# Optimization experiments

Measured on AMD Instinct MI355X. Metric: run time of the kernel, lower is better.

## Reference

```python
import jax, jax.numpy as jnp
import numpy as np

B, S, D = 4, 4096, 2048  # batch, seq, hidden
E, R, K = 8, 16, 2       # n_experts, rank, top_k


def setup_inputs() -> dict:
    key = jax.random.key(0)
    k1, k2, k3, k4 = jax.random.split(key, 4)
    x = jax.random.normal(k1, (B, S, D), dtype=jnp.float32)
    router_w = jax.random.normal(k2, (E, D), dtype=jnp.float32) * 0.02  # nn.Linear weight (out,in)
    experts_down = jax.random.normal(k3, (E, D, R), dtype=jnp.float32) * 0.01
    experts_up = jax.random.normal(k4, (E, R, D), dtype=jnp.float32) * 0.01
    return {"x": x, "router_w": router_w, "experts_down": experts_down, "experts_up": experts_up}


def reference(x, router_w, experts_down, experts_up):
    E_ = router_w.shape[0]
    # router sees detached x (torch: self.router(x.detach()))
    logits = jnp.einsum('bsd,ed->bse', jax.lax.stop_gradient(x), router_w)
    w, idx = jax.lax.top_k(logits, K)          # (B,S,K)
    w = jax.nn.softmax(w, axis=-1)
    # combined per-token, per-expert routing weight; zero for non-selected experts
    w_full = jnp.sum(jax.nn.one_hot(idx, E_, dtype=x.dtype) * w[..., None], axis=2)  # (B,S,E)
    # rank-space activations per expert: (B,S,E,R) -- small (R=16)
    h = jnp.einsum('bsd,edr->bser', x, experts_down)
    # fuse routing weight into rank space, then up-project and sum over experts
    out = x + jnp.einsum('bser,bse,erd->bsd', h, w_full, experts_up)
    return out
```

## Files before the change

kernel.cpp:

```cpp
#include <hip/hip_runtime.h>
#include <hip/hip_bf16.h>

#define MTOK 16384
#define DDIM 2048
#define NEXP 8
#define RNK 16
#define NC 128
#define NW 160
#define LOGIT0 128
#define KSPLIT 2
#define KLEN (DDIM / KSPLIT)
#define NT (KLEN / 64)

typedef __attribute__((ext_vector_type(8))) short bf16x8;
typedef __attribute__((ext_vector_type(4))) short short4v;
typedef __attribute__((ext_vector_type(4))) float f32x4;

typedef __attribute__((address_space(1))) const void gv_t;
typedef __attribute__((address_space(3))) void lv_t;

__device__ __forceinline__ short f2b(float f) {
  unsigned u = __float_as_uint(f);
  u += 0x7fffu + ((u >> 16) & 1u);
  return (short)(u >> 16);
}
__device__ __forceinline__ float b2f(short s) {
  return __uint_as_float(((unsigned)(unsigned short)s) << 16);
}

__global__ __launch_bounds__(256) void prep_k(const float* __restrict__ rw,
                                              const float* __restrict__ down,
                                              const float* __restrict__ up,
                                              short* __restrict__ WdT,
                                              short* __restrict__ UT) {
  int i = blockIdx.x * 256 + threadIdx.x;
  const int NWD = NW * DDIM;
  const int NUT = DDIM * NC;
  if (i < NWD) {
    int n = i / DDIM, k = i % DDIM;
    int s = (k >> 3) & 7;
    int src_k = (k & ~0x3F) | ((s ^ (n & 7)) << 3) | (k & 7);
    float v = 0.f;
    if (n < NC)             v = down[((n >> 4) * DDIM + src_k) * RNK + (n & 15)];
    else if (n < NC + NEXP) v = rw[(n - NC) * DDIM + src_k];
    WdT[i] = f2b(v);
  } else if (i < NWD + NUT) {
    int u = i - NWD;
    int d = u >> 7, c = u & 127;
    UT[u] = f2b(up[((c >> 4) * RNK + (c & 15)) * DDIM + d]);
  }
}

__global__ __launch_bounds__(256, 2) void gemm1_k(const float* __restrict__ X,
                                                  const short* __restrict__ WdT,
                                                  short* __restrict__ Hp) {
  __shared__ short Al[2][64][72];
  __shared__ short Bl[2][160 * 64];
  const int tid = threadIdx.x;
  const int lane = tid & 63;
  const int w = tid >> 6;
  const int gm0 = blockIdx.x * 64;
  const int ks = blockIdx.y;
  const int kb = ks * KLEN;
  const int wr = (w & 1) * 32;
  const int wc = (w >> 1) * 80;
  const int lr = lane & 15;
  const int lk = (lane >> 4) * 8;

  f32x4 acc[2][5];
#pragma unroll
  for (int m = 0; m < 2; ++m)
#pragma unroll
    for (int n = 0; n < 5; ++n) acc[m][n] = (f32x4){0.f, 0.f, 0.f, 0.f};

  float4 aR[4];

  auto loadA = [&](int k0) {
#pragma unroll
    for (int i2 = 0; i2 < 4; ++i2) {
      int f = tid + 256 * i2;
      int row = f >> 4, c4 = f & 15;
      aR[i2] = *(const float4*)(X + (size_t)(gm0 + row) * DDIM + k0 + c4 * 4);
    }
  };
  auto issueB = [&](int buf, int k0) {
#pragma unroll
    for (int j = 0; j < 5; ++j) {
      int u = (w * 5 + j) * 64 + lane;
      const short* g = WdT + (size_t)(u >> 3) * DDIM + k0 + (u & 7) * 8;
      short* l = &Bl[buf][(w * 5 + j) * 512];
      __builtin_amdgcn_global_load_lds((gv_t*)g, (lv_t*)l, 16, 0, 0);
    }
  };
  auto writeA = [&](int buf) {
#pragma unroll
    for (int i2 = 0; i2 < 4; ++i2) {
      int f = tid + 256 * i2;
      int row = f >> 4, c4 = f & 15;
      short4v v;
      v.x = f2b(aR[i2].x); v.y = f2b(aR[i2].y);
      v.z = f2b(aR[i2].z); v.w = f2b(aR[i2].w);
      *(short4v*)&Al[buf][row][c4 * 4] = v;
    }
  };
  auto compute = [&](int buf) {
#pragma unroll
    for (int kk2 = 0; kk2 < 2; ++kk2) {
      const int kk = kk2 * 32;
      bf16x8 a[2], b[5];
#pragma unroll
      for (int m = 0; m < 2; ++m)
        a[m] = *(const bf16x8*)&Al[buf][wr + m * 16 + lr][kk + lk];
#pragma unroll
      for (int n = 0; n < 5; ++n) {
        int row = wc + n * 16 + lr;
        int sl = ((kk >> 3) + (lane >> 4)) ^ (row & 7);
        b[n] = *(const bf16x8*)&Bl[buf][row * 64 + sl * 8];
      }
#pragma unroll
      for (int m = 0; m < 2; ++m)
#pragma unroll
        for (int n = 0; n < 5; ++n)
          acc[m][n] = __builtin_amdgcn_mfma_f32_16x16x32_bf16(a[m], b[n], acc[m][n], 0, 0, 0);
    }
  };

  loadA(kb);
  issueB(0, kb);
  writeA(0);
  __syncthreads();
  for (int t = 0; t < NT; ++t) {
    const int cur = t & 1, nxt = cur ^ 1;
    if (t + 1 < NT) {
      loadA(kb + (t + 1) * 64);
      issueB(nxt, kb + (t + 1) * 64);
    }
    compute(cur);
    if (t + 1 < NT) writeA(nxt);
    __syncthreads();
  }

  short* Hq = Hp + (size_t)ks * MTOK * NW;
  const int cr = (lane >> 4) * 4;
#pragma unroll
  for (int m = 0; m < 2; ++m)
#pragma unroll
    for (int n = 0; n < 5; ++n)
#pragma unroll
      for (int r = 0; r < 4; ++r) {
        int row = gm0 + wr + m * 16 + cr + r;
        int col = wc + n * 16 + lr;
        Hq[(size_t)row * NW + col] = f2b(acc[m][n][r]);
      }
}

__global__ __launch_bounds__(256) void route_k(const short* __restrict__ Hp,
                                               short* __restrict__ Hw) {
  __shared__ float wv[64][8];
  const int tid = threadIdx.x;
  const int t0 = blockIdx.x * 64;
  const short* H0 = Hp;
  const short* H1 = Hp + (size_t)MTOK * NW;
  if (tid < 64) {
    int t = t0 + tid;
    uint4 l0 = *(const uint4*)(H0 + (size_t)t * NW + LOGIT0);
    uint4 l1 = *(const uint4*)(H1 + (size_t)t * NW + LOGIT0);
    const short* p0 = (const short*)&l0;
    const short* p1 = (const short*)&l1;
    float b0 = -1e30f, b1 = -1e30f;
    int i0 = 0, i1 = 0;
#pragma unroll
    for (int e = 0; e < 8; ++e) {
      float v = b2f(p0[e]) + b2f(p1[e]);
      if (v > b0) { b1 = b0; i1 = i0; b0 = v; i0 = e; }
      else if (v > b1) { b1 = v; i1 = e; }
    }
    float ex = __expf(b1 - b0);
    float inv = 1.f / (1.f + ex);
#pragma unroll
    for (int e = 0; e < 8; ++e)
      wv[tid][e] = (e == i0) ? inv : ((e == i1) ? ex * inv : 0.f);
  }
  __syncthreads();
  const int t = tid >> 2, q = tid & 3;
  const short* a0 = H0 + (size_t)(t0 + t) * NW + q * 32;
  const short* a1 = H1 + (size_t)(t0 + t) * NW + q * 32;
  short* o = Hw + (size_t)(t0 + t) * NC + q * 32;
#pragma unroll
  for (int j = 0; j < 4; ++j) {
    uint4 v0 = *(const uint4*)(a0 + j * 8);
    uint4 v1 = *(const uint4*)(a1 + j * 8);
    const short* s0 = (const short*)&v0;
    const short* s1 = (const short*)&v1;
    short r[8];
    int cbase = q * 32 + j * 8;
#pragma unroll
    for (int e2 = 0; e2 < 8; ++e2) {
      float h = b2f(s0[e2]) + b2f(s1[e2]);
      r[e2] = f2b(h * wv[t][(cbase + e2) >> 4]);
    }
    *(uint4*)(o + j * 8) = *(uint4*)r;
  }
}

__global__ __launch_bounds__(256) void gemm2_k(const short* __restrict__ Hw,
                                               const short* __restrict__ UT,
                                               const float* __restrict__ X,
                                               float* __restrict__ Out) {
  __shared__ short Al[128][136];
  __shared__ short Bl[64][136];
  const int tid = threadIdx.x;
  const int lane = tid & 63;
  const int w = tid >> 6;
  const int gm0 = blockIdx.x * 128;
  const int n0 = blockIdx.y * 64;
  const int lr = lane & 15;
  const int lk = (lane >> 4) * 8;

#pragma unroll
  for (int i = 0; i < 8; ++i) {
    int f = tid + 256 * i;
    int row = f >> 4, c8 = f & 15;
    *(uint4*)&Al[row][c8 * 8] = *(const uint4*)(Hw + (size_t)(gm0 + row) * NC + c8 * 8);
  }
#pragma unroll
  for (int i = 0; i < 4; ++i) {
    int f = tid + 256 * i;
    int row = f >> 4, c8 = f & 15;
    *(uint4*)&Bl[row][c8 * 8] = *(const uint4*)(UT + (size_t)(n0 + row) * NC + c8 * 8);
  }
  __syncthreads();

  f32x4 acc[2][4];
#pragma unroll
  for (int m = 0; m < 2; ++m)
#pragma unroll
    for (int n = 0; n < 4; ++n) acc[m][n] = (f32x4){0.f, 0.f, 0.f, 0.f};

#pragma unroll
  for (int ks = 0; ks < 4; ++ks) {
    const int kk = ks * 32;
    bf16x8 a[2], b[4];
#pragma unroll
    for (int m = 0; m < 2; ++m) a[m] = *(const bf16x8*)&Al[w * 32 + m * 16 + lr][kk + lk];
#pragma unroll
    for (int n = 0; n < 4; ++n) b[n] = *(const bf16x8*)&Bl[n * 16 + lr][kk + lk];
#pragma unroll
    for (int m = 0; m < 2; ++m)
#pragma unroll
      for (int n = 0; n < 4; ++n)
        acc[m][n] = __builtin_amdgcn_mfma_f32_16x16x32_bf16(a[m], b[n], acc[m][n], 0, 0, 0);
  }

  const int cr = (lane >> 4) * 4;
#pragma unroll
  for (int m = 0; m < 2; ++m)
#pragma unroll
    for (int n = 0; n < 4; ++n)
#pragma unroll
      for (int r = 0; r < 4; ++r) {
        int row = gm0 + w * 32 + m * 16 + cr + r;
        int col = n0 + n * 16 + lr;
        size_t idx = (size_t)row * DDIM + col;
        Out[idx] = X[idx] + acc[m][n][r];
      }
}

extern "C" void kernel_launch(void* const* d_in, const int* in_sizes, int n_in,
                              void* d_out, int out_size, void* d_ws, size_t ws_size,
                              hipStream_t stream) {
  const float* x    = (const float*)d_in[0];
  const float* rw   = (const float*)d_in[1];
  const float* down = (const float*)d_in[2];
  const float* up   = (const float*)d_in[3];
  float* out = (float*)d_out;

  char* ws = (char*)d_ws;
  short* WdT = (short*)ws;
  short* UT  = (short*)(ws + 655360);
  short* Hp  = (short*)(ws + 1179648);
  short* Hw  = (short*)(ws + 11665408);

  prep_k<<<2304, 256, 0, stream>>>(rw, down, up, WdT, UT);
  gemm1_k<<<dim3(MTOK / 64, KSPLIT), 256, 0, stream>>>(x, WdT, Hp);
  route_k<<<MTOK / 64, 256, 0, stream>>>(Hp, Hw);
  gemm2_k<<<dim3(MTOK / 128, DDIM / 64), 256, 0, stream>>>(Hw, UT, x, out);
}
```

Baseline: 92.35 us.

## Deepen gemm1 prefetch pipeline and vectorize gemm2 epilogue via LDS staging

gemm1 now prefetches A tiles two K-steps ahead into a second register set and uses explicit vmcnt/lgkmcnt waits with raw barriers instead of __syncthreads. Its launch bounds are raised from 2 to 4 blocks per SIMD to allow more occupancy. The gemm2 epilogue stages accumulators through LDS so the residual add and store use coalesced float4 accesses instead of scalar strided ones. The trade-off is more register pressure from the doubled A prefetch under the tighter launch bound, plus hand-counted waitcnt values that must stay in sync with the exact load counts.

```diff
diff --git a/kernel.cpp b/kernel.cpp
--- a/kernel.cpp
+++ b/kernel.cpp
@@ -51,7 +51,7 @@
   }
 }
 
-__global__ __launch_bounds__(256, 2) void gemm1_k(const float* __restrict__ X,
+__global__ __launch_bounds__(256, 4) void gemm1_k(const float* __restrict__ X,
                                                   const short* __restrict__ WdT,
                                                   short* __restrict__ Hp) {
   __shared__ short Al[2][64][72];
@@ -73,14 +73,14 @@
 #pragma unroll
     for (int n = 0; n < 5; ++n) acc[m][n] = (f32x4){0.f, 0.f, 0.f, 0.f};
 
-  float4 aR[4];
-
-  auto loadA = [&](int k0) {
+  float4 aR[2][4];
+
+  auto loadA = [&](int k0, int s) {
 #pragma unroll
     for (int i2 = 0; i2 < 4; ++i2) {
       int f = tid + 256 * i2;
       int row = f >> 4, c4 = f & 15;
-      aR[i2] = *(const float4*)(X + (size_t)(gm0 + row) * DDIM + k0 + c4 * 4);
+      aR[s][i2] = *(const float4*)(X + (size_t)(gm0 + row) * DDIM + k0 + c4 * 4);
     }
   };
   auto issueB = [&](int buf, int k0) {
@@ -92,14 +92,14 @@
       __builtin_amdgcn_global_load_lds((gv_t*)g, (lv_t*)l, 16, 0, 0);
     }
   };
-  auto writeA = [&](int buf) {
+  auto writeA = [&](int buf, int s) {
 #pragma unroll
     for (int i2 = 0; i2 < 4; ++i2) {
       int f = tid + 256 * i2;
       int row = f >> 4, c4 = f & 15;
       short4v v;
-      v.x = f2b(aR[i2].x); v.y = f2b(aR[i2].y);
-      v.z = f2b(aR[i2].z); v.w = f2b(aR[i2].w);
+      v.x = f2b(aR[s][i2].x); v.y = f2b(aR[s][i2].y);
+      v.z = f2b(aR[s][i2].z); v.w = f2b(aR[s][i2].w);
       *(short4v*)&Al[buf][row][c4 * 4] = v;
     }
   };
@@ -125,19 +125,37 @@
     }
   };
 
-  loadA(kb);
+  loadA(kb, 0);
   issueB(0, kb);
-  writeA(0);
-  __syncthreads();
+  loadA(kb + 64, 1);
+  issueB(1, kb + 64);
+  asm volatile("s_waitcnt vmcnt(12)" ::: "memory");
+  __builtin_amdgcn_sched_barrier(0);
+  writeA(0, 0);
+  asm volatile("s_waitcnt vmcnt(7)" ::: "memory");
+  asm volatile("s_waitcnt lgkmcnt(0)" ::: "memory");
+  __builtin_amdgcn_sched_barrier(0);
+  __builtin_amdgcn_s_barrier();
+
+#pragma unroll
   for (int t = 0; t < NT; ++t) {
-    const int cur = t & 1, nxt = cur ^ 1;
+    if (t + 2 < NT) loadA(kb + (t + 2) * 64, t & 1);
+    compute(t & 1);
+    asm volatile("s_waitcnt lgkmcnt(0)" ::: "memory");
+    __builtin_amdgcn_s_barrier();
+    __builtin_amdgcn_sched_barrier(0);
+    if (t + 2 < NT) issueB(t & 1, kb + (t + 2) * 64);
     if (t + 1 < NT) {
-      loadA(kb + (t + 1) * 64);
-      issueB(nxt, kb + (t + 1) * 64);
-    }
-    compute(cur);
-    if (t + 1 < NT) writeA(nxt);
-    __syncthreads();
+      if (t + 2 < NT)
+        asm volatile("s_waitcnt vmcnt(7)" ::: "memory");
+      else
+        asm volatile("s_waitcnt vmcnt(0)" ::: "memory");
+      __builtin_amdgcn_sched_barrier(0);
+      writeA((t + 1) & 1, (t + 1) & 1);
+      asm volatile("s_waitcnt lgkmcnt(0)" ::: "memory");
+      __builtin_amdgcn_sched_barrier(0);
+    }
+    __builtin_amdgcn_s_barrier();
   }
 
   short* Hq = Hp + (size_t)ks * MTOK * NW;
@@ -252,18 +270,26 @@
         acc[m][n] = __builtin_amdgcn_mfma_f32_16x16x32_bf16(a[m], b[n], acc[m][n], 0, 0, 0);
   }
 
+  float* eps = (float*)&Al[0][0] + w * 2176;
   const int cr = (lane >> 4) * 4;
 #pragma unroll
   for (int m = 0; m < 2; ++m)
 #pragma unroll
     for (int n = 0; n < 4; ++n)
 #pragma unroll
-      for (int r = 0; r < 4; ++r) {
-        int row = gm0 + w * 32 + m * 16 + cr + r;
-        int col = n0 + n * 16 + lr;
-        size_t idx = (size_t)row * DDIM + col;
-        Out[idx] = X[idx] + acc[m][n][r];
-      }
+      for (int r = 0; r < 4; ++r)
+        eps[(m * 16 + cr + r) * 68 + n * 16 + lr] = acc[m][n][r];
+
+#pragma unroll
+  for (int j = 0; j < 8; ++j) {
+    int c = lane + 64 * j;
+    int rl = c >> 4, c4 = c & 15;
+    float4 v = *(const float4*)&eps[rl * 68 + c4 * 4];
+    size_t idx = (size_t)(gm0 + w * 32 + rl) * DDIM + n0 + c4 * 4;
+    const float4 xv = *(const float4*)(X + idx);
+    v.x += xv.x; v.y += xv.y; v.z += xv.z; v.w += xv.w;
+    *(float4*)(Out + idx) = v;
+  }
 }
 
 extern "C" void kernel_launch(void* const* d_in, const int* in_sizes, int n_in,
```

Result: faster. 87.00 us (-5.8%).
